# Performance work log

Hardware: AMD Instinct MI355X
Metric: run time of the kernel (lower is better)

## Reference

```python
import jax, jax.numpy as jnp
import numpy as np

ALPHA = 0.3  # Keras LeakyReLU default

def leaky_relu(x):
    return jnp.where(x > 0, x, ALPHA * x)

def lstm_last_h(x, Wx, Wh, b):
    # x: [B,T,F]; returns final hidden state [B,H]. Keras LSTMCell gate order i,f,g,o.
    B = x.shape[0]
    H = Wh.shape[0]
    xz = jnp.einsum('btf,fg->btg', x, Wx) + b  # precompute input projections [B,T,4H]
    def step(carry, xz_t):
        h, c = carry
        z = xz_t + h @ Wh
        i, f, g, o = jnp.split(z, 4, axis=-1)
        c = jax.nn.sigmoid(f) * c + jax.nn.sigmoid(i) * jnp.tanh(g)
        h = jax.nn.sigmoid(o) * jnp.tanh(c)
        return (h, c), None
    init = (jnp.zeros((B, H), x.dtype), jnp.zeros((B, H), x.dtype))
    (h, _), _ = jax.lax.scan(step, init, jnp.swapaxes(xz, 0, 1))
    return h

def causal_conv1d(x, k, b, stride):
    # Keras 'causal': left-pad by (kernel-1), then valid conv with stride.
    pad = k.shape[0] - 1
    xp = jnp.pad(x, ((0, 0), (pad, 0), (0, 0)))
    y = jax.lax.conv_general_dilated(xp, k, (stride,), 'VALID',
                                     dimension_numbers=('NWC', 'WIO', 'NWC'))
    return y + b

def setup_inputs() -> dict:
    key = jax.random.key(0)
    ks = jax.random.split(key, 10)
    B, T, F, H = 1024, 512, 51, 256
    s = 0.05  # weight scale for numerical stability
    x = jax.random.normal(ks[0], (B, T, F), jnp.float32)
    Wx = jax.random.normal(ks[1], (F, 4 * H), jnp.float32) * s
    Wh = jax.random.normal(ks[2], (H, 4 * H), jnp.float32) * s
    b_lstm = jnp.zeros((4 * H,), jnp.float32)
    k1 = jax.random.normal(ks[3], (5, F, 64), jnp.float32) * s
    b1 = jnp.zeros((64,), jnp.float32)
    k2 = jax.random.normal(ks[4], (5, 64, 128), jnp.float32) * s
    b2 = jnp.zeros((128,), jnp.float32)
    # conv out length: ceil(T/2)=256, then ceil(256/2)=128 -> flatten 128*128=16384; +H=16640
    Wd = jax.random.normal(ks[5], (16384 + H, 1), jnp.float32) * s
    bd = jnp.zeros((1,), jnp.float32)
    return {"x": x, "Wx": Wx, "Wh": Wh, "b_lstm": b_lstm,
            "k1": k1, "b1": b1, "k2": k2, "b2": b2, "Wd": Wd, "bd": bd}

def reference(x, Wx, Wh, b_lstm, k1, b1, k2, b2, Wd, bd):
    # Line A: RNN(LSTMCell(256)) -> last h -> LeakyReLU (dropout = identity at inference)
    a = leaky_relu(lstm_last_h(x, Wx, Wh, b_lstm))  # [B,256]
    # Line B: two causal stride-2 convs with LeakyReLU, then flatten
    h1 = leaky_relu(causal_conv1d(x, k1, b1, 2))    # [B,256,64]
    h2 = leaky_relu(causal_conv1d(h1, k2, b2, 2))   # [B,128,128]
    bfeat = h2.reshape(h2.shape[0], -1)             # [B,16384]
    feat = jnp.concatenate([a, bfeat], axis=-1)     # [B,16640]
    return feat @ Wd + bd                           # [B,1]
```

## Files before the change

kernel.cpp:

```cpp
#include <hip/hip_runtime.h>
#include <hip/hip_fp16.h>
#include <stdint.h>

#define ALPHA 0.3f
#define NSL 12

__device__ __forceinline__ float leaky(float v) { return v > 0.0f ? v : ALPHA * v; }
__device__ __forceinline__ float sigm(float v)  { return 1.0f / (1.0f + __expf(-v)); }
__device__ __forceinline__ float tanh_fast(float v) { return 1.0f - 2.0f / (1.0f + __expf(2.0f * v)); }
__device__ __forceinline__ __half2 u2h(unsigned u) { union { unsigned u; __half2 h; } c; c.u = u; return c.h; }

__global__ __launch_bounds__(256) void pack_w(
    const float* __restrict__ Wh, const float* __restrict__ Wx,
    unsigned* __restrict__ Whp, unsigned* __restrict__ Wxp) {
    int idx = blockIdx.x * 256 + threadIdx.x;
    if (idx < 128 * 1024) {
        int kp = idx >> 10, rem = idx & 1023;
        int j = rem >> 2, g = rem & 3;
        int col = g * 256 + j;
        float a = Wh[(2 * kp) * 1024 + col];
        float b = Wh[(2 * kp + 1) * 1024 + col];
        Whp[idx] = (unsigned)__half_as_ushort(__float2half(a))
                 | ((unsigned)__half_as_ushort(__float2half(b)) << 16);
    } else {
        int i = idx - 128 * 1024;
        int fp = i >> 10, rem = i & 1023;
        int j = rem >> 2, g = rem & 3;
        int col = g * 256 + j;
        float a = Wx[(2 * fp) * 1024 + col];
        float b = (2 * fp + 1 < 51) ? Wx[(2 * fp + 1) * 1024 + col] : 0.0f;
        Wxp[i] = (unsigned)__half_as_ushort(__float2half(a))
               | ((unsigned)__half_as_ushort(__float2half(b)) << 16);
    }
}

__global__ __launch_bounds__(256) void conv_kernel(
    const float* __restrict__ x,
    const float* __restrict__ k1, const float* __restrict__ b1,
    const float* __restrict__ k2, const float* __restrict__ b2,
    const float* __restrict__ Wd, const float* __restrict__ bd,
    float* __restrict__ out) {
    extern __shared__ unsigned char smem[];
    float* h1s = (float*)smem;
    float* xs  = (float*)(smem + 65536);

    const int tid = threadIdx.x;
    const int b   = blockIdx.x;
    const float* xb = x + (size_t)b * (512 * 51);

    const int c1g = tid & 15;
    const int t1g = tid >> 4;
    float4 b1v = *(const float4*)&b1[c1g * 4];

    #pragma unroll
    for (int chunk = 0; chunk < 2; ++chunk) {
        const int tb   = chunk ? 128 : 0;
        const int rb   = chunk ? 252 : 0;
        const int rows = chunk ? 259 : 255;
        {
            const float* src = xb + rb * 51;
            int total = rows * 51;
            int n4 = total >> 2;
            const float4* s4 = (const float4*)src;
            float4* d4 = (float4*)xs;
            for (int i = tid; i < n4; i += 256) d4[i] = s4[i];
            for (int i = (n4 << 2) + tid; i < total; i += 256) xs[i] = src[i];
        }
        __syncthreads();

        float acc[8][4];
        #pragma unroll
        for (int i = 0; i < 8; ++i) { acc[i][0]=0.f; acc[i][1]=0.f; acc[i][2]=0.f; acc[i][3]=0.f; }

        for (int w = 0; w < 5; ++w) {
            for (int f = 0; f < 51; ++f) {
                float4 wt = *(const float4*)&k1[(w * 51 + f) * 64 + c1g * 4];
                #pragma unroll
                for (int i = 0; i < 8; ++i) {
                    int t1 = tb + t1g * 8 + i;
                    int r = 2 * t1 + w - 4;
                    if (r >= rb) {
                        float a = xs[(r - rb) * 51 + f];
                        acc[i][0] += a * wt.x; acc[i][1] += a * wt.y;
                        acc[i][2] += a * wt.z; acc[i][3] += a * wt.w;
                    }
                }
            }
        }
        #pragma unroll
        for (int i = 0; i < 8; ++i) {
            int t1 = tb + t1g * 8 + i;
            float* dst = &h1s[t1 * 64 + c1g * 4];
            dst[0] = leaky(acc[i][0] + b1v.x);
            dst[1] = leaky(acc[i][1] + b1v.y);
            dst[2] = leaky(acc[i][2] + b1v.z);
            dst[3] = leaky(acc[i][3] + b1v.w);
        }
        __syncthreads();
    }

    const int c2g = tid & 31;
    const int t2g = tid >> 5;
    float acc2[16][4];
    #pragma unroll
    for (int i = 0; i < 16; ++i) { acc2[i][0]=0.f; acc2[i][1]=0.f; acc2[i][2]=0.f; acc2[i][3]=0.f; }

    for (int w = 0; w < 5; ++w) {
        for (int c1 = 0; c1 < 64; ++c1) {
            float4 wt = *(const float4*)&k2[(w * 64 + c1) * 128 + c2g * 4];
            #pragma unroll
            for (int i = 0; i < 16; ++i) {
                int t2 = t2g * 16 + i;
                int r = 2 * t2 + w - 4;
                if (r >= 0) {
                    float a = h1s[r * 64 + c1];
                    acc2[i][0] += a * wt.x; acc2[i][1] += a * wt.y;
                    acc2[i][2] += a * wt.z; acc2[i][3] += a * wt.w;
                }
            }
        }
    }

    float4 b2v = *(const float4*)&b2[c2g * 4];
    float p = 0.f;
    #pragma unroll
    for (int i = 0; i < 16; ++i) {
        int t2 = t2g * 16 + i;
        float4 wd = *(const float4*)&Wd[256 + t2 * 128 + c2g * 4];
        p += leaky(acc2[i][0] + b2v.x) * wd.x;
        p += leaky(acc2[i][1] + b2v.y) * wd.y;
        p += leaky(acc2[i][2] + b2v.z) * wd.z;
        p += leaky(acc2[i][3] + b2v.w) * wd.w;
    }

    float* red = xs;
    __syncthreads();
    red[tid] = p;
    __syncthreads();
    for (int s = 128; s > 0; s >>= 1) {
        if (tid < s) red[tid] += red[tid + s];
        __syncthreads();
    }
    if (tid == 0) out[b] = red[0] + bd[0];
}

__global__ __launch_bounds__(256) void lstm_kernel(
    const float* __restrict__ x,
    const uint4*  __restrict__ Whp,
    const uint4*  __restrict__ Wxp,
    const float*  __restrict__ bl,
    const float*  __restrict__ Wd,
    float* __restrict__ out) {
    extern __shared__ unsigned char smem[];
    unsigned* wx_l = (unsigned*)smem;
    unsigned* wh_l = (unsigned*)(smem + 106496);
    unsigned* h16  = (unsigned*)(smem + 106496 + NSL * 4096);
    unsigned* xt16 = (unsigned*)(smem + 106496 + NSL * 4096 + 2048);

    const int j  = threadIdx.x;
    const int b0 = blockIdx.x * 4;

    {
        uint4* d = (uint4*)wx_l;
        for (int i = j; i < 26 * 256; i += 256) d[i] = Wxp[i];
        uint4* dw = (uint4*)wh_l;
        for (int i = j; i < NSL * 256; i += 256) dw[i] = Whp[i];
    }
    h16[j] = 0; h16[j + 256] = 0;
    if (j < 104) xt16[j] = 0;
    const float bz0 = bl[j], bz1 = bl[j + 256], bz2 = bl[j + 512], bz3 = bl[j + 768];
    float cc[4] = {0.f, 0.f, 0.f, 0.f};
    float hn[4] = {0.f, 0.f, 0.f, 0.f};
    unsigned short* h16s  = (unsigned short*)h16;
    unsigned short* xt16s = (unsigned short*)xt16;

    const int fx = j >> 2, rx = j & 3;
    const float* xptr = x + ((size_t)(b0 + rx) * 512) * 51 + fx;
    float xpre = (j < 204) ? xptr[0] : 0.0f;
    __syncthreads();

    for (int t = 0; t < 512; ++t) {
        if (j < 204)
            xt16s[(fx >> 1) * 8 + rx * 2 + (fx & 1)] = __half_as_ushort(__float2half(xpre));
        __syncthreads();

        float xnext = 0.0f;
        if (j < 204 && t + 1 < 512) xnext = xptr[(t + 1) * 51];

        __half2 acc[4][4];
        #pragma unroll
        for (int r = 0; r < 4; ++r)
            #pragma unroll
            for (int g = 0; g < 4; ++g) acc[r][g] = u2h(0u);

        #pragma unroll 2
        for (int fp = 0; fp < 26; ++fp) {
            uint4 wq = ((const uint4*)wx_l)[fp * 256 + j];
            uint4 hq = *(const uint4*)&xt16[fp * 4];
            __half2 xv[4] = {u2h(hq.x), u2h(hq.y), u2h(hq.z), u2h(hq.w)};
            __half2 wv[4] = {u2h(wq.x), u2h(wq.y), u2h(wq.z), u2h(wq.w)};
            #pragma unroll
            for (int r = 0; r < 4; ++r)
                #pragma unroll
                for (int g = 0; g < 4; ++g)
                    acc[r][g] = __hfma2(xv[r], wv[g], acc[r][g]);
        }

        #pragma unroll 4
        for (int kp = 0; kp < NSL; ++kp) {
            uint4 wq = ((const uint4*)wh_l)[kp * 256 + j];
            uint4 hq = *(const uint4*)&h16[kp * 4];
            __half2 hv[4] = {u2h(hq.x), u2h(hq.y), u2h(hq.z), u2h(hq.w)};
            __half2 wv[4] = {u2h(wq.x), u2h(wq.y), u2h(wq.z), u2h(wq.w)};
            #pragma unroll
            for (int r = 0; r < 4; ++r)
                #pragma unroll
                for (int g = 0; g < 4; ++g)
                    acc[r][g] = __hfma2(hv[r], wv[g], acc[r][g]);
        }
        #pragma unroll 8
        for (int kp = NSL; kp < 128; ++kp) {
            uint4 wq = Whp[kp * 256 + j];
            uint4 hq = *(const uint4*)&h16[kp * 4];
            __half2 hv[4] = {u2h(hq.x), u2h(hq.y), u2h(hq.z), u2h(hq.w)};
            __half2 wv[4] = {u2h(wq.x), u2h(wq.y), u2h(wq.z), u2h(wq.w)};
            #pragma unroll
            for (int r = 0; r < 4; ++r)
                #pragma unroll
                for (int g = 0; g < 4; ++g)
                    acc[r][g] = __hfma2(hv[r], wv[g], acc[r][g]);
        }

        #pragma unroll
        for (int r = 0; r < 4; ++r) {
            float zi = __low2float(acc[r][0]) + __high2float(acc[r][0]) + bz0;
            float zf = __low2float(acc[r][1]) + __high2float(acc[r][1]) + bz1;
            float zg = __low2float(acc[r][2]) + __high2float(acc[r][2]) + bz2;
            float zo = __low2float(acc[r][3]) + __high2float(acc[r][3]) + bz3;
            float iv = sigm(zi);
            float fv = sigm(zf);
            float gv = tanh_fast(zg);
            float ov = sigm(zo);
            cc[r] = fv * cc[r] + iv * gv;
            hn[r] = ov * tanh_fast(cc[r]);
        }
        __syncthreads();
        xpre = xnext;
        #pragma unroll
        for (int r = 0; r < 4; ++r)
            h16s[(j >> 1) * 8 + r * 2 + (j & 1)] = __half_as_ushort(__float2half(hn[r]));
    }

    const float pw = Wd[j];
    float p0 = leaky(hn[0]) * pw;
    float p1 = leaky(hn[1]) * pw;
    float p2 = leaky(hn[2]) * pw;
    float p3 = leaky(hn[3]) * pw;
    float* red = (float*)wh_l;
    __syncthreads();
    *(float4*)&red[j * 4] = make_float4(p0, p1, p2, p3);
    __syncthreads();
    for (int s = 128; s > 0; s >>= 1) {
        if (j < s) {
            float4 a = *(const float4*)&red[j * 4];
            float4 c = *(const float4*)&red[(j + s) * 4];
            a.x += c.x; a.y += c.y; a.z += c.z; a.w += c.w;
            *(float4*)&red[j * 4] = a;
        }
        __syncthreads();
    }
    if (j < 4) out[b0 + j] += red[j];
}

extern "C" void kernel_launch(void* const* d_in, const int* in_sizes, int n_in,
                              void* d_out, int out_size, void* d_ws, size_t ws_size,
                              hipStream_t stream) {
    const float* x   = (const float*)d_in[0];
    const float* Wx  = (const float*)d_in[1];
    const float* Wh  = (const float*)d_in[2];
    const float* bl  = (const float*)d_in[3];
    const float* k1  = (const float*)d_in[4];
    const float* b1  = (const float*)d_in[5];
    const float* k2  = (const float*)d_in[6];
    const float* b2  = (const float*)d_in[7];
    const float* Wd  = (const float*)d_in[8];
    const float* bd  = (const float*)d_in[9];
    float* out = (float*)d_out;

    unsigned* Whp = (unsigned*)d_ws;
    unsigned* Wxp = Whp + 128 * 1024;

    const int conv_smem = 65536 + 13212 * 4;
    const int lstm_smem = 106496 + NSL * 4096 + 2048 + 416;

    hipFuncSetAttribute((const void*)conv_kernel,
                        hipFuncAttributeMaxDynamicSharedMemorySize, conv_smem);
    hipFuncSetAttribute((const void*)lstm_kernel,
                        hipFuncAttributeMaxDynamicSharedMemorySize, lstm_smem);

    pack_w<<<616, 256, 0, stream>>>(Wh, Wx, Whp, Wxp);
    conv_kernel<<<1024, 256, conv_smem, stream>>>(x, k1, b1, k2, b2, Wd, bd, out);
    lstm_kernel<<<256, 256, lstm_smem, stream>>>(x, (const uint4*)Whp, (const uint4*)Wxp,
                                                 bl, Wd, out);
}
```

Baseline: 6.436 ms.

## Split LSTM recurrent reduction across two thread groups with LDS exchange

The LSTM block grows from 256 to 512 threads, and each half handles half of the K dimension for both the input and the recurrent matmul. Partial sums for the other half's batch rows are exchanged through shared memory, and each group then computes the gates for two batch rows. The shared-memory-resident Wh slice is dropped in favour of register-prefetched streaming of Wh from global memory with an 8-deep buffer. The aim is to halve the serial per-step critical path and hide load latency, at the cost of an extra LDS exchange per step and higher register pressure.

```diff
diff --git a/kernel.cpp b/kernel.cpp
--- a/kernel.cpp
+++ b/kernel.cpp
@@ -3,7 +3,6 @@
 #include <stdint.h>
 
 #define ALPHA 0.3f
-#define NSL 12
 
 __device__ __forceinline__ float leaky(float v) { return v > 0.0f ? v : ALPHA * v; }
 __device__ __forceinline__ float sigm(float v)  { return 1.0f / (1.0f + __expf(-v)); }
@@ -55,10 +54,10 @@
     #pragma unroll
     for (int chunk = 0; chunk < 2; ++chunk) {
         const int tb   = chunk ? 128 : 0;
-        const int rb   = chunk ? 252 : 0;
+        const int rb_  = chunk ? 252 : 0;
         const int rows = chunk ? 259 : 255;
         {
-            const float* src = xb + rb * 51;
+            const float* src = xb + rb_ * 51;
             int total = rows * 51;
             int n4 = total >> 2;
             const float4* s4 = (const float4*)src;
@@ -79,8 +78,8 @@
                 for (int i = 0; i < 8; ++i) {
                     int t1 = tb + t1g * 8 + i;
                     int r = 2 * t1 + w - 4;
-                    if (r >= rb) {
-                        float a = xs[(r - rb) * 51 + f];
+                    if (r >= rb_) {
+                        float a = xs[(r - rb_) * 51 + f];
                         acc[i][0] += a * wt.x; acc[i][1] += a * wt.y;
                         acc[i][2] += a * wt.z; acc[i][3] += a * wt.w;
                     }
@@ -144,7 +143,48 @@
     if (tid == 0) out[b] = red[0] + bd[0];
 }
 
-__global__ __launch_bounds__(256) void lstm_kernel(
+__device__ __forceinline__ void fma16(__half2 (&acc)[4][4], uint4 wq, uint4 hq) {
+    __half2 hv[4] = {u2h(hq.x), u2h(hq.y), u2h(hq.z), u2h(hq.w)};
+    __half2 wv[4] = {u2h(wq.x), u2h(wq.y), u2h(wq.z), u2h(wq.w)};
+    #pragma unroll
+    for (int r = 0; r < 4; ++r)
+        #pragma unroll
+        for (int g = 0; g < 4; ++g)
+            acc[r][g] = __hfma2(hv[r], wv[g], acc[r][g]);
+}
+
+__device__ __forceinline__ void pub2(const __half2 (&a0)[4], const __half2 (&a1)[4],
+                                     float* rb, int tid) {
+    #pragma unroll
+    for (int g = 0; g < 4; ++g) {
+        rb[g * 516 + tid]       = __low2float(a0[g]) + __high2float(a0[g]);
+        rb[(4 + g) * 516 + tid] = __low2float(a1[g]) + __high2float(a1[g]);
+    }
+}
+
+__device__ __forceinline__ void gate2(const __half2 (&a0)[4], const __half2 (&a1)[4],
+                                      const float* rb, int or_tid,
+                                      float bz0, float bz1, float bz2, float bz3,
+                                      float (&cc)[2], float (&hn)[2],
+                                      unsigned short* h16s, int j, int mr0) {
+    #pragma unroll
+    for (int rr = 0; rr < 2; ++rr) {
+        const __half2* a = rr ? a1 : a0;
+        float zi = __low2float(a[0]) + __high2float(a[0]) + rb[(rr * 4 + 0) * 516 + or_tid] + bz0;
+        float zf = __low2float(a[1]) + __high2float(a[1]) + rb[(rr * 4 + 1) * 516 + or_tid] + bz1;
+        float zg = __low2float(a[2]) + __high2float(a[2]) + rb[(rr * 4 + 2) * 516 + or_tid] + bz2;
+        float zo = __low2float(a[3]) + __high2float(a[3]) + rb[(rr * 4 + 3) * 516 + or_tid] + bz3;
+        float iv = sigm(zi);
+        float fv = sigm(zf);
+        float gv = tanh_fast(zg);
+        float ov = sigm(zo);
+        cc[rr] = fv * cc[rr] + iv * gv;
+        hn[rr] = ov * tanh_fast(cc[rr]);
+        h16s[(j >> 1) * 8 + (mr0 + rr) * 2 + (j & 1)] = __half_as_ushort(__float2half(hn[rr]));
+    }
+}
+
+__global__ __launch_bounds__(512) void lstm_kernel(
     const float* __restrict__ x,
     const uint4*  __restrict__ Whp,
     const uint4*  __restrict__ Wxp,
@@ -153,39 +193,42 @@
     float* __restrict__ out) {
     extern __shared__ unsigned char smem[];
     unsigned* wx_l = (unsigned*)smem;
-    unsigned* wh_l = (unsigned*)(smem + 106496);
-    unsigned* h16  = (unsigned*)(smem + 106496 + NSL * 4096);
-    unsigned* xt16 = (unsigned*)(smem + 106496 + NSL * 4096 + 2048);
-
-    const int j  = threadIdx.x;
-    const int b0 = blockIdx.x * 4;
+    unsigned* h16  = (unsigned*)(smem + 106496);
+    unsigned* xt16 = (unsigned*)(smem + 108544);
+    float*    rb   = (float*)   (smem + 108960);
+
+    const int tid = threadIdx.x;
+    const int j   = tid & 255;
+    const int grp = tid >> 8;
+    const int b0  = blockIdx.x * 4;
+    const int k0  = grp * 64;
+    const int f0  = grp * 13;
+    const int mr0 = grp * 2;
 
     {
         uint4* d = (uint4*)wx_l;
-        for (int i = j; i < 26 * 256; i += 256) d[i] = Wxp[i];
-        uint4* dw = (uint4*)wh_l;
-        for (int i = j; i < NSL * 256; i += 256) dw[i] = Whp[i];
-    }
-    h16[j] = 0; h16[j + 256] = 0;
-    if (j < 104) xt16[j] = 0;
+        for (int i = tid; i < 26 * 256; i += 512) d[i] = Wxp[i];
+    }
+    h16[tid] = 0;
+    if (tid < 104) xt16[tid] = 0;
     const float bz0 = bl[j], bz1 = bl[j + 256], bz2 = bl[j + 512], bz3 = bl[j + 768];
-    float cc[4] = {0.f, 0.f, 0.f, 0.f};
-    float hn[4] = {0.f, 0.f, 0.f, 0.f};
+    float cc[2] = {0.f, 0.f};
+    float hn[2] = {0.f, 0.f};
     unsigned short* h16s  = (unsigned short*)h16;
     unsigned short* xt16s = (unsigned short*)xt16;
 
-    const int fx = j >> 2, rx = j & 3;
+    const int fx = tid >> 2, rx = tid & 3;
     const float* xptr = x + ((size_t)(b0 + rx) * 512) * 51 + fx;
-    float xpre = (j < 204) ? xptr[0] : 0.0f;
+    float xpre = (tid < 204) ? xptr[0] : 0.0f;
     __syncthreads();
 
     for (int t = 0; t < 512; ++t) {
-        if (j < 204)
+        if (tid < 204)
             xt16s[(fx >> 1) * 8 + rx * 2 + (fx & 1)] = __half_as_ushort(__float2half(xpre));
         __syncthreads();
 
         float xnext = 0.0f;
-        if (j < 204 && t + 1 < 512) xnext = xptr[(t + 1) * 51];
+        if (tid < 204 && t + 1 < 512) xnext = xptr[(t + 1) * 51];
 
         __half2 acc[4][4];
         #pragma unroll
@@ -193,83 +236,64 @@
             #pragma unroll
             for (int g = 0; g < 4; ++g) acc[r][g] = u2h(0u);
 
-        #pragma unroll 2
-        for (int fp = 0; fp < 26; ++fp) {
+        const uint4* wbase = Whp + (size_t)k0 * 256 + j;
+        uint4 wbuf[8];
+        #pragma unroll
+        for (int i = 0; i < 8; ++i) wbuf[i] = wbase[i * 256];
+
+        #pragma unroll
+        for (int ff = 0; ff < 13; ++ff) {
+            int fp = f0 + ff;
             uint4 wq = ((const uint4*)wx_l)[fp * 256 + j];
             uint4 hq = *(const uint4*)&xt16[fp * 4];
-            __half2 xv[4] = {u2h(hq.x), u2h(hq.y), u2h(hq.z), u2h(hq.w)};
-            __half2 wv[4] = {u2h(wq.x), u2h(wq.y), u2h(wq.z), u2h(wq.w)};
+            fma16(acc, wq, hq);
+        }
+
+        for (int kb = 0; kb < 56; kb += 8) {
             #pragma unroll
-            for (int r = 0; r < 4; ++r)
-                #pragma unroll
-                for (int g = 0; g < 4; ++g)
-                    acc[r][g] = __hfma2(xv[r], wv[g], acc[r][g]);
-        }
-
-        #pragma unroll 4
-        for (int kp = 0; kp < NSL; ++kp) {
-            uint4 wq = ((const uint4*)wh_l)[kp * 256 + j];
-            uint4 hq = *(const uint4*)&h16[kp * 4];
-            __half2 hv[4] = {u2h(hq.x), u2h(hq.y), u2h(hq.z), u2h(hq.w)};
-            __half2 wv[4] = {u2h(wq.x), u2h(wq.y), u2h(wq.z), u2h(wq.w)};
-            #pragma unroll
-            for (int r = 0; r < 4; ++r)
-                #pragma unroll
-                for (int g = 0; g < 4; ++g)
-                    acc[r][g] = __hfma2(hv[r], wv[g], acc[r][g]);
-        }
-        #pragma unroll 8
-        for (int kp = NSL; kp < 128; ++kp) {
-            uint4 wq = Whp[kp * 256 + j];
-            uint4 hq = *(const uint4*)&h16[kp * 4];
-            __half2 hv[4] = {u2h(hq.x), u2h(hq.y), u2h(hq.z), u2h(hq.w)};
-            __half2 wv[4] = {u2h(wq.x), u2h(wq.y), u2h(wq.z), u2h(wq.w)};
-            #pragma unroll
-            for (int r = 0; r < 4; ++r)
-                #pragma unroll
-                for (int g = 0; g < 4; ++g)
-                    acc[r][g] = __hfma2(hv[r], wv[g], acc[r][g]);
-        }
-
-        #pragma unroll
-        for (int r = 0; r < 4; ++r) {
-            float zi = __low2float(acc[r][0]) + __high2float(acc[r][0]) + bz0;
-            float zf = __low2float(acc[r][1]) + __high2float(acc[r][1]) + bz1;
-            float zg = __low2float(acc[r][2]) + __high2float(acc[r][2]) + bz2;
-            float zo = __low2float(acc[r][3]) + __high2float(acc[r][3]) + bz3;
-            float iv = sigm(zi);
-            float fv = sigm(zf);
-            float gv = tanh_fast(zg);
-            float ov = sigm(zo);
-            cc[r] = fv * cc[r] + iv * gv;
-            hn[r] = ov * tanh_fast(cc[r]);
-        }
-        __syncthreads();
+            for (int kk = 0; kk < 8; ++kk) {
+                uint4 wq = wbuf[kk];
+                wbuf[kk] = wbase[(kb + 8 + kk) * 256];
+                uint4 hq = *(const uint4*)&h16[(k0 + kb + kk) * 4];
+                fma16(acc, wq, hq);
+            }
+        }
+        #pragma unroll
+        for (int kk = 0; kk < 8; ++kk) {
+            uint4 wq = wbuf[kk];
+            uint4 hq = *(const uint4*)&h16[(k0 + 56 + kk) * 4];
+            fma16(acc, wq, hq);
+        }
+
+        if (grp == 0) pub2(acc[2], acc[3], rb, tid);
+        else          pub2(acc[0], acc[1], rb, tid);
+        __syncthreads();
+
+        if (grp == 0) gate2(acc[0], acc[1], rb, tid ^ 256, bz0, bz1, bz2, bz3,
+                            cc, hn, h16s, j, mr0);
+        else          gate2(acc[2], acc[3], rb, tid ^ 256, bz0, bz1, bz2, bz3,
+                            cc, hn, h16s, j, mr0);
         xpre = xnext;
-        #pragma unroll
-        for (int r = 0; r < 4; ++r)
-            h16s[(j >> 1) * 8 + r * 2 + (j & 1)] = __half_as_ushort(__float2half(hn[r]));
     }
 
     const float pw = Wd[j];
     float p0 = leaky(hn[0]) * pw;
     float p1 = leaky(hn[1]) * pw;
-    float p2 = leaky(hn[2]) * pw;
-    float p3 = leaky(hn[3]) * pw;
-    float* red = (float*)wh_l;
-    __syncthreads();
-    *(float4*)&red[j * 4] = make_float4(p0, p1, p2, p3);
-    __syncthreads();
-    for (int s = 128; s > 0; s >>= 1) {
-        if (j < s) {
-            float4 a = *(const float4*)&red[j * 4];
-            float4 c = *(const float4*)&red[(j + s) * 4];
-            a.x += c.x; a.y += c.y; a.z += c.z; a.w += c.w;
-            *(float4*)&red[j * 4] = a;
-        }
-        __syncthreads();
-    }
-    if (j < 4) out[b0 + j] += red[j];
+    __syncthreads();
+    rb[(mr0 + 0) * 516 + j] = p0;
+    rb[(mr0 + 1) * 516 + j] = p1;
+    __syncthreads();
+    const int rid = tid >> 7;
+    const int l   = tid & 127;
+    float v = rb[rid * 516 + l] + rb[rid * 516 + l + 128];
+    rb[rid * 516 + l] = v;
+    __syncthreads();
+    if (l < 64) {
+        v = rb[rid * 516 + l] + rb[rid * 516 + l + 64];
+        #pragma unroll
+        for (int off = 32; off; off >>= 1) v += __shfl_down(v, off, 64);
+        if (l == 0) out[b0 + rid] += v;
+    }
 }
 
 extern "C" void kernel_launch(void* const* d_in, const int* in_sizes, int n_in,
@@ -291,7 +315,7 @@
     unsigned* Wxp = Whp + 128 * 1024;
 
     const int conv_smem = 65536 + 13212 * 4;
-    const int lstm_smem = 106496 + NSL * 4096 + 2048 + 416;
+    const int lstm_smem = 106496 + 2048 + 416 + 16512;
 
     hipFuncSetAttribute((const void*)conv_kernel,
                         hipFuncAttributeMaxDynamicSharedMemorySize, conv_smem);
@@ -300,6 +324,6 @@
 
     pack_w<<<616, 256, 0, stream>>>(Wh, Wx, Whp, Wxp);
     conv_kernel<<<1024, 256, conv_smem, stream>>>(x, k1, b1, k2, b2, Wd, bd, out);
-    lstm_kernel<<<256, 256, lstm_smem, stream>>>(x, (const uint4*)Whp, (const uint4*)Wxp,
+    lstm_kernel<<<256, 512, lstm_smem, stream>>>(x, (const uint4*)Whp, (const uint4*)Wxp,
                                                  bl, Wd, out);
 }
```

Measured after the change: 9.317 ms. +44.8%, slower.
